# Kernel tuning notes

Hardware: AMD Instinct MI355X
Metric: run time of the kernel (lower is better)

The kernel has to match this reference:

```python
import jax, jax.numpy as jnp
import numpy as np

D_MODEL = 512
N_HEADS = 8
D_HEAD = D_MODEL // N_HEADS
EPS = 1e-5


def layer_norm(x, g, b):
    mu = jnp.mean(x, axis=-1, keepdims=True)
    var = jnp.mean(jnp.square(x - mu), axis=-1, keepdims=True)
    return (x - mu) * jax.lax.rsqrt(var + EPS) * g + b


def setup_inputs() -> dict:
    key = jax.random.key(0)
    ks = jax.random.split(key, 8)
    B, L, D = 2, 4096, D_MODEL
    x = jax.random.normal(ks[0], (B, L, D), dtype=jnp.float32)
    # monotonically increasing event timestamps (hours)
    timestamps = jnp.sort(jax.random.uniform(ks[1], (B, L), dtype=jnp.float32) * 1000.0, axis=-1)
    mask = jnp.ones((B, L), dtype=jnp.float32)
    s = 0.02
    return {
        "x": x,
        "timestamps": timestamps,
        "mask": mask,
        "ln1_g": jnp.ones((D,), jnp.float32),
        "ln1_b": jnp.zeros((D,), jnp.float32),
        "w_qkv": jax.random.normal(ks[2], (3 * D, D), jnp.float32) * s,
        "w_out": jax.random.normal(ks[3], (D, D), jnp.float32) * s,
        "decay_rate": jnp.ones((N_HEADS,), jnp.float32) * 0.01,
        "ln2_g": jnp.ones((D,), jnp.float32),
        "ln2_b": jnp.zeros((D,), jnp.float32),
        "w_ff1": jax.random.normal(ks[4], (4 * D, D), jnp.float32) * s,
        "w_ff2": jax.random.normal(ks[5], (D, 4 * D), jnp.float32) * s,
    }


def reference(x, timestamps, mask, ln1_g, ln1_b, w_qkv, w_out, decay_rate, ln2_g, ln2_b, w_ff1, w_ff2):
    B, L, D = x.shape
    H, dh = N_HEADS, D_HEAD
    scale = dh ** (-0.5)

    xn = layer_norm(x, ln1_g, ln1_b)
    qkv = (xn @ w_qkv.T).reshape(B, L, 3, H, dh).transpose(2, 0, 3, 1, 4)  # [3,B,H,L,dh]
    q, k, v = qkv[0], qkv[1], qkv[2]

    attn = jnp.einsum("bhid,bhjd->bhij", q, k) * scale  # [B,H,L,L]

    # temporal-decay bias
    t_diff = jnp.abs(timestamps[:, None, :, None] - timestamps[:, None, None, :]) / 24.0  # [B,1,L,L]
    decay = jax.nn.softplus(decay_rate)[None, :, None, None]  # [1,H,1,1]
    attn = attn - decay * t_diff

    # causal mask
    causal = jnp.triu(jnp.ones((L, L), dtype=bool), k=1)
    attn = jnp.where(causal[None, None], -jnp.inf, attn)

    # padding mask over keys
    pad = (mask == 0)[:, None, None, :]  # [B,1,1,L]
    attn = jnp.where(pad, -jnp.inf, attn)

    attn = jax.nn.softmax(attn, axis=-1)
    out = jnp.einsum("bhij,bhjd->bhid", attn, v).transpose(0, 2, 1, 3).reshape(B, L, D)

    x = x + out @ w_out.T
    h = layer_norm(x, ln2_g, ln2_b)
    x = x + jax.nn.silu(h @ w_ff1.T) @ w_ff2.T
    return x
```

## Files before the change

### kernel.cpp

```cpp
#include <hip/hip_runtime.h>
#include <hip/hip_bf16.h>
#include <cmath>


#define L_SEQ 4096
#define D_MODEL 512
#define N_HEADS 8
#define D_HEAD 64
#define QKV_LD 1536

typedef __attribute__((ext_vector_type(8))) short bf16x8;
typedef __attribute__((ext_vector_type(4))) float f32x4;
typedef __attribute__((ext_vector_type(4))) unsigned u32x4;

__device__ __forceinline__ __hip_bfloat16 f2bf(float v) { return __float2bfloat16(v); }

__device__ __forceinline__ void gl_lds16(const __hip_bfloat16* g, __hip_bfloat16* l) {
  __builtin_amdgcn_global_load_lds((__attribute__((address_space(1))) void*)g,
                                   (__attribute__((address_space(3))) void*)l, 16, 0, 0);
}

__global__ __launch_bounds__(256) void cvt4_kernel(const float* __restrict__ s0, __hip_bfloat16* __restrict__ d0,
                                                   const float* __restrict__ s1, __hip_bfloat16* __restrict__ d1,
                                                   const float* __restrict__ s2, __hip_bfloat16* __restrict__ d2,
                                                   const float* __restrict__ s3, __hip_bfloat16* __restrict__ d3) {
  const int i = blockIdx.x * 256 + threadIdx.x;
  const float* s;
  __hip_bfloat16* d;
  int off;
  if (i < 196608) { s = s0; d = d0; off = i; }
  else if (i < 262144) { s = s1; d = d1; off = i - 196608; }
  else if (i < 524288) { s = s2; d = d2; off = i - 262144; }
  else { s = s3; d = d3; off = i - 524288; }
  const float4 v = ((const float4*)s)[off];
  d[4 * off + 0] = f2bf(v.x);
  d[4 * off + 1] = f2bf(v.y);
  d[4 * off + 2] = f2bf(v.z);
  d[4 * off + 3] = f2bf(v.w);
}

__global__ __launch_bounds__(256) void bias_kernel(const float* __restrict__ ts,
                                                   const float* __restrict__ mask,
                                                   const float* __restrict__ decay_rate,
                                                   float* __restrict__ biasH) {
  const int idx = blockIdx.x * 256 + threadIdx.x;
  const int col = idx & 4095;
  const int h = (idx >> 12) & 7;
  const int b = idx >> 15;
  const float LOG2E = 1.4426950408889634f;
  const float dfac = log1pf(expf(decay_rate[h])) * (1.0f / 24.0f) * LOG2E;
  const float m = mask[b * 4096 + col];
  biasH[idx] = dfac * ts[b * 4096 + col] + (m != 0.f ? 0.f : -1e30f);
}

__global__ __launch_bounds__(256) void ln_kernel(const float* __restrict__ x,
                                                 const float* __restrict__ g,
                                                 const float* __restrict__ b,
                                                 __hip_bfloat16* __restrict__ out) {
  const int row = blockIdx.x;
  const int t = threadIdx.x;
  const float* xr = x + (size_t)row * D_MODEL;
  float v0 = xr[t];
  float v1 = xr[t + 256];
  float s = v0 + v1;
  float qq = v0 * v0 + v1 * v1;
  for (int off = 32; off > 0; off >>= 1) {
    s += __shfl_xor(s, off);
    qq += __shfl_xor(qq, off);
  }
  __shared__ float red[8];
  const int wid = t >> 6;
  if ((t & 63) == 0) { red[wid] = s; red[4 + wid] = qq; }
  __syncthreads();
  s = red[0] + red[1] + red[2] + red[3];
  qq = red[4] + red[5] + red[6] + red[7];
  const float mu = s * (1.0f / 512.0f);
  const float var = fmaxf(qq * (1.0f / 512.0f) - mu * mu, 0.0f);
  const float rstd = rsqrtf(var + 1e-5f);
  __hip_bfloat16* orow = out + (size_t)row * D_MODEL;
  orow[t] = f2bf((v0 - mu) * rstd * g[t] + b[t]);
  orow[t + 256] = f2bf((v1 - mu) * rstd * g[t + 256] + b[t + 256]);
}

__global__ __launch_bounds__(256) void vtrans_kernel(const __hip_bfloat16* __restrict__ qkv,
                                                     __hip_bfloat16* __restrict__ vt) {
  const int gid = blockIdx.x * 256 + threadIdx.x;
  const int l = gid & 4095;
  const int bg = gid >> 12;
  const int b = bg >> 6, g = bg & 63;
  const int h = g >> 3, dg = (g & 7) * 8;
  const __hip_bfloat16* src = qkv + (size_t)(b * L_SEQ + l) * QKV_LD + 1024 + h * 64 + dg;
  bf16x8 v = *(const bf16x8*)src;
  const int kin = l & 63;
  const int sl = (kin & 0x23) | ((kin & 0x10) >> 2) | ((kin & 0x0c) << 1);
  const size_t dbase = (size_t)((b * 8 + h) * 64 + dg) * L_SEQ + (l & ~63) + sl;
  for (int j = 0; j < 8; j++)
    vt[dbase + (size_t)j * L_SEQ] = ((const __hip_bfloat16*)&v)[j];
}

template <int EPI>
__global__ __launch_bounds__(256) void gemm_kernel(const __hip_bfloat16* __restrict__ A,
                                                   const __hip_bfloat16* __restrict__ B,
                                                   int M, int N, int K,
                                                   const float* __restrict__ aux,
                                                   void* __restrict__ C) {
  __shared__ __align__(16) __hip_bfloat16 As[2][128 * 32];
  __shared__ __align__(16) __hip_bfloat16 Bs[2][128 * 32];
  const int tid = threadIdx.x;
  const int lane = tid & 63, w = tid >> 6;
  const int m0 = blockIdx.y * 128, n0 = blockIdx.x * 128;
  const int wm = (w >> 1) * 64, wn = (w & 1) * 64;
  const int r = lane & 15, q = lane >> 4;

  f32x4 acc[4][4];
  const f32x4 zz = {0.f, 0.f, 0.f, 0.f};
  for (int i = 0; i < 4; i++)
    for (int j = 0; j < 4; j++) acc[i][j] = zz;

  const int c0 = tid, c1 = 256 + tid;
  const int row0 = c0 >> 2, kb0 = (c0 & 3) * 8;
  const int row1 = c1 >> 2, kb1 = (c1 & 3) * 8;

#define GEMM_STAGE(k0, buf)                                                     \
  do {                                                                          \
    gl_lds16(A + (size_t)(m0 + row0) * K + ((k0) + kb0), &As[buf][c0 * 8]);     \
    gl_lds16(B + (size_t)(n0 + row0) * K + ((k0) + kb0), &Bs[buf][c0 * 8]);     \
    gl_lds16(A + (size_t)(m0 + row1) * K + ((k0) + kb1), &As[buf][c1 * 8]);     \
    gl_lds16(B + (size_t)(n0 + row1) * K + ((k0) + kb1), &Bs[buf][c1 * 8]);     \
  } while (0)

  GEMM_STAGE(0, 0);
  const int niter = K >> 5;
  for (int it = 0; it < niter; it++) {
    const int cur = it & 1;
    if (it + 1 < niter) {
      GEMM_STAGE((it + 1) << 5, cur ^ 1);
      asm volatile("s_waitcnt vmcnt(4)" ::: "memory");
    } else {
      asm volatile("s_waitcnt vmcnt(0)" ::: "memory");
    }
    __builtin_amdgcn_s_barrier();
    bf16x8 af[4], bfr[4];
    for (int mi = 0; mi < 4; mi++)
      af[mi] = *(const bf16x8*)(&As[cur][(wm + mi * 16 + r) * 32 + q * 8]);
    for (int ni = 0; ni < 4; ni++)
      bfr[ni] = *(const bf16x8*)(&Bs[cur][(wn + ni * 16 + r) * 32 + q * 8]);
    for (int mi = 0; mi < 4; mi++)
      for (int ni = 0; ni < 4; ni++)
        acc[mi][ni] = __builtin_amdgcn_mfma_f32_16x16x32_bf16(af[mi], bfr[ni], acc[mi][ni], 0, 0, 0);
    __builtin_amdgcn_s_barrier();
  }
#undef GEMM_STAGE

  for (int mi = 0; mi < 4; mi++)
    for (int ni = 0; ni < 4; ni++)
      for (int j = 0; j < 4; j++) {
        const int gm = m0 + wm + mi * 16 + q * 4 + j;
        const int gn = n0 + wn + ni * 16 + r;
        float v = acc[mi][ni][j];
        const size_t idx = (size_t)gm * N + gn;
        if (EPI == 0) {
          ((__hip_bfloat16*)C)[idx] = f2bf(v);
        } else if (EPI == 1) {
          ((float*)C)[idx] = v + aux[idx];
        } else if (EPI == 2) {
          v = v / (1.0f + expf(-v));
          ((__hip_bfloat16*)C)[idx] = f2bf(v);
        } else {
          ((float*)C)[idx] = v + aux[idx];
        }
      }
}

__device__ __forceinline__ void stage_kv(int w, int lane, int key0,
                                         const __hip_bfloat16* __restrict__ Kg,
                                         const __hip_bfloat16* __restrict__ Vg,
                                         __hip_bfloat16* Ks, __hip_bfloat16* Vs) {
  const int row_in = lane >> 3;
  const int cs = (lane & 7) ^ row_in;
#pragma unroll
  for (int ii = 0; ii < 2; ii++) {
    const int i = w * 2 + ii;
    const int row = i * 8 + row_in;
    gl_lds16(Kg + (size_t)(key0 + row) * QKV_LD + cs * 8, Ks + i * 512 + lane * 8);
    gl_lds16(Vg + (size_t)row * L_SEQ + key0 + cs * 8, Vs + i * 512 + lane * 8);
  }
}

template <bool CAUSAL>
__device__ __forceinline__ void attn_tile(int key0, int lw0, int r, int q,
                                          const __hip_bfloat16* Ks,
                                          const __hip_bfloat16* Vs,
                                          const float* __restrict__ biasHp,
                                          float scale2,
                                          const bf16x8& qf0, const bf16x8& qf1,
                                          f32x4* o, float& ls) {
  const int r7 = r & 7;
  const f32x4 zz = {0.f, 0.f, 0.f, 0.f};
  f32x4 bias4[4];
#pragma unroll
  for (int hc = 0; hc < 4; hc++)
    bias4[hc] = *(const f32x4*)(biasHp + key0 + hc * 16 + q * 4);
  f32x4 s[4];
  __builtin_amdgcn_s_setprio(1);
#pragma unroll
  for (int hc = 0; hc < 4; hc++) {
    const __hip_bfloat16* kr = Ks + (hc * 16 + r) * 64;
    bf16x8 k0 = *(const bf16x8*)(kr + ((q ^ r7) * 8));
    bf16x8 k1 = *(const bf16x8*)(kr + (((q + 4) ^ r7) * 8));
    f32x4 a = zz;
    a = __builtin_amdgcn_mfma_f32_16x16x32_bf16(k0, qf0, a, 0, 0, 0);
    a = __builtin_amdgcn_mfma_f32_16x16x32_bf16(k1, qf1, a, 0, 0, 0);
    s[hc] = a;
  }
  __builtin_amdgcn_s_setprio(0);
  float p[4][4];
  float sum = 0.f;
#pragma unroll
  for (int hc = 0; hc < 4; hc++)
#pragma unroll
    for (int j = 0; j < 4; j++) {
      const float v = fmaf(s[hc][j], scale2, bias4[hc][j]);
      float pv = exp2f(v);
      if (CAUSAL) pv = (key0 + hc * 16 + q * 4 + j <= lw0 + r) ? pv : 0.f;
      p[hc][j] = pv;
      sum += pv;
    }
  ls += sum;
  bf16x8 pa[2];
#pragma unroll
  for (int kc = 0; kc < 2; kc++) {
    u32x4 pw;
    unsigned w0, w1, w2, w3;
    asm("v_cvt_pk_bf16_f32 %0, %1, %2" : "=v"(w0) : "v"(p[2 * kc][0]), "v"(p[2 * kc][1]));
    asm("v_cvt_pk_bf16_f32 %0, %1, %2" : "=v"(w1) : "v"(p[2 * kc][2]), "v"(p[2 * kc][3]));
    asm("v_cvt_pk_bf16_f32 %0, %1, %2" : "=v"(w2) : "v"(p[2 * kc + 1][0]), "v"(p[2 * kc + 1][1]));
    asm("v_cvt_pk_bf16_f32 %0, %1, %2" : "=v"(w3) : "v"(p[2 * kc + 1][2]), "v"(p[2 * kc + 1][3]));
    pw[0] = w0; pw[1] = w1; pw[2] = w2; pw[3] = w3;
    pa[kc] = *(bf16x8*)&pw;
  }
  __builtin_amdgcn_s_setprio(1);
#pragma unroll
  for (int kc = 0; kc < 2; kc++)
#pragma unroll
    for (int c = 0; c < 4; c++) {
      const __hip_bfloat16* vr = Vs + (c * 16 + r) * 64 + (((kc * 4 + q) ^ r7) * 8);
      bf16x8 vf = *(const bf16x8*)vr;
      o[c] = __builtin_amdgcn_mfma_f32_16x16x32_bf16(pa[kc], vf, o[c], 0, 0, 0);
    }
  __builtin_amdgcn_s_setprio(0);
}

__global__ __launch_bounds__(256, 4) void attn_kernel(const __hip_bfloat16* __restrict__ qkv,
                                                      const __hip_bfloat16* __restrict__ vt,
                                                      const float* __restrict__ biasH,
                                                      __hip_bfloat16* __restrict__ out) {
  const int blk = blockIdx.x;
  const int g = blk >> 4;
  const int bh = blk & 15;
  const int gm = g >> 4, gk = g & 15;
  const int qi = (gm == 0) ? gk : (gm == 1) ? 63 - gk : (gm == 2) ? 16 + gk : 47 - gk;
  const int b = bh >> 3, h = bh & 7;
  const int l0 = qi * 64;
  const int tid = threadIdx.x, lane = tid & 63, w = tid >> 6;
  const int lw0 = l0 + w * 16;
  const int r = lane & 15, q = lane >> 4;

  __shared__ __align__(16) __hip_bfloat16 Ksm[2][64 * 64];
  __shared__ __align__(16) __hip_bfloat16 Vsm[2][64 * 64];

  const float LOG2E = 1.4426950408889634f;
  const float scale2 = 0.125f * LOG2E;

  const __hip_bfloat16* Kg = qkv + (size_t)b * L_SEQ * QKV_LD + 512 + h * 64;
  const __hip_bfloat16* Vg = vt + (size_t)bh * 64 * L_SEQ;
  const float* biasHp = biasH + (size_t)bh * L_SEQ;

  stage_kv(w, lane, 0, Kg, Vg, Ksm[0], Vsm[0]);

  bf16x8 qf0, qf1;
  {
    const __hip_bfloat16* qrow = qkv + (size_t)(b * L_SEQ + lw0 + r) * QKV_LD + h * 64 + q * 8;
    qf0 = *(const bf16x8*)qrow;
    qf1 = *(const bf16x8*)(qrow + 32);
  }

  const f32x4 zz = {0.f, 0.f, 0.f, 0.f};
  f32x4 o[4];
  for (int c = 0; c < 4; c++) o[c] = zz;
  float ls = 0.f;

  const int ntiles = qi + 1;
  for (int t = 0; t < ntiles; t++) {
    const int cur = t & 1;
    if (t + 1 < ntiles) {
      stage_kv(w, lane, (t + 1) << 6, Kg, Vg, Ksm[cur ^ 1], Vsm[cur ^ 1]);
      asm volatile("s_waitcnt vmcnt(4)" ::: "memory");
    } else {
      asm volatile("s_waitcnt vmcnt(0)" ::: "memory");
    }
    __builtin_amdgcn_s_barrier();
    if (t < ntiles - 1)
      attn_tile<false>(t << 6, lw0, r, q, Ksm[cur], Vsm[cur], biasHp, scale2, qf0, qf1, o, ls);
    else
      attn_tile<true>(t << 6, lw0, r, q, Ksm[cur], Vsm[cur], biasHp, scale2, qf0, qf1, o, ls);
    __builtin_amdgcn_s_barrier();
  }

  float lt = ls;
  lt += __shfl_xor(lt, 16);
  lt += __shfl_xor(lt, 32);
  const float invr = 1.0f / lt;
  float invj[4];
  for (int j = 0; j < 4; j++) invj[j] = __shfl(invr, q * 4 + j);
  for (int c = 0; c < 4; c++)
    for (int j = 0; j < 4; j++) {
      const int rowg = lw0 + q * 4 + j;
      out[(size_t)(b * L_SEQ + rowg) * D_MODEL + h * 64 + c * 16 + r] = f2bf(o[c][j] * invj[j]);
    }
}

extern "C" void kernel_launch(void* const* d_in, const int* in_sizes, int n_in,
                              void* d_out, int out_size, void* d_ws, size_t ws_size,
                              hipStream_t stream) {
  const float* x = (const float*)d_in[0];
  const float* ts = (const float*)d_in[1];
  const float* mask = (const float*)d_in[2];
  const float* ln1_g = (const float*)d_in[3];
  const float* ln1_b = (const float*)d_in[4];
  const float* w_qkv = (const float*)d_in[5];
  const float* w_out = (const float*)d_in[6];
  const float* decay = (const float*)d_in[7];
  const float* ln2_g = (const float*)d_in[8];
  const float* ln2_b = (const float*)d_in[9];
  const float* w_ff1 = (const float*)d_in[10];
  const float* w_ff2 = (const float*)d_in[11];

  char* ws = (char*)d_ws;
  __hip_bfloat16* wqkv_b = (__hip_bfloat16*)(ws + 0);
  __hip_bfloat16* wout_b = (__hip_bfloat16*)(ws + 1572864);
  __hip_bfloat16* wff1_b = (__hip_bfloat16*)(ws + 2097152);
  __hip_bfloat16* wff2_b = (__hip_bfloat16*)(ws + 4194304);
  __hip_bfloat16* xn = (__hip_bfloat16*)(ws + 6291456);
  __hip_bfloat16* vt = (__hip_bfloat16*)(ws + 6291456);
  __hip_bfloat16* qkv = (__hip_bfloat16*)(ws + 14680064);
  __hip_bfloat16* attnout = (__hip_bfloat16*)(ws + 39845888);
  __hip_bfloat16* h = attnout;
  __hip_bfloat16* ff1out = (__hip_bfloat16*)(ws + 6291456);
  float* x2 = (float*)(ws + 48234496);
  float* biasH = (float*)(ws + 48234496);
  float* out = (float*)d_out;

  const int M = 2 * L_SEQ;

  cvt4_kernel<<<dim3(3072), dim3(256), 0, stream>>>(w_qkv, wqkv_b, w_out, wout_b,
                                                    w_ff1, wff1_b, w_ff2, wff2_b);
  bias_kernel<<<dim3(256), dim3(256), 0, stream>>>(ts, mask, decay, biasH);

  ln_kernel<<<dim3(M), dim3(256), 0, stream>>>(x, ln1_g, ln1_b, xn);
  gemm_kernel<0><<<dim3(12, 64), dim3(256), 0, stream>>>(xn, wqkv_b, M, 1536, 512, nullptr, qkv);
  vtrans_kernel<<<dim3(2048), dim3(256), 0, stream>>>(qkv, vt);
  attn_kernel<<<dim3(1024), dim3(256), 0, stream>>>(qkv, vt, biasH, attnout);
  gemm_kernel<1><<<dim3(4, 64), dim3(256), 0, stream>>>(attnout, wout_b, M, 512, 512, x, x2);
  ln_kernel<<<dim3(M), dim3(256), 0, stream>>>(x2, ln2_g, ln2_b, h);
  gemm_kernel<2><<<dim3(16, 64), dim3(256), 0, stream>>>(h, wff1_b, M, 2048, 512, nullptr, ff1out);
  gemm_kernel<3><<<dim3(4, 64), dim3(256), 0, stream>>>(ff1out, wff2_b, M, 512, 2048, x2, out);
}
```

Before: 307.3 us.

## Pair causal query tiles per attention block and add 64-row residual GEMM

The attention kernel now gives each block two query tiles, qi and 63-qi, and processes them back to back. Every block therefore does the same total amount of causal work, and the grid shrinks from 1024 to 512 blocks with launch bounds relaxed to 2 blocks per CU. A new 64x128-tile GEMM with a residual epilogue replaces the 128-tile version for the out-projection and FF2, which doubles the block count on these narrow N=512 GEMMs to fill more CUs. The trade-off is fewer attention blocks in flight, and a first-tile loop that prefetches tile 0 on its final iteration for the second pass.

```diff
diff --git a/kernel.cpp b/kernel.cpp
--- a/kernel.cpp
+++ b/kernel.cpp
@@ -161,14 +161,73 @@
         const size_t idx = (size_t)gm * N + gn;
         if (EPI == 0) {
           ((__hip_bfloat16*)C)[idx] = f2bf(v);
-        } else if (EPI == 1) {
-          ((float*)C)[idx] = v + aux[idx];
-        } else if (EPI == 2) {
+        } else {
           v = v / (1.0f + expf(-v));
           ((__hip_bfloat16*)C)[idx] = f2bf(v);
-        } else {
-          ((float*)C)[idx] = v + aux[idx];
         }
+      }
+}
+
+__global__ __launch_bounds__(256) void gemm_res64_kernel(const __hip_bfloat16* __restrict__ A,
+                                                         const __hip_bfloat16* __restrict__ B,
+                                                         int M, int N, int K,
+                                                         const float* __restrict__ aux,
+                                                         float* __restrict__ C) {
+  __shared__ __align__(16) __hip_bfloat16 As[2][64 * 32];
+  __shared__ __align__(16) __hip_bfloat16 Bs[2][128 * 32];
+  const int tid = threadIdx.x;
+  const int lane = tid & 63, w = tid >> 6;
+  const int m0 = blockIdx.y * 64, n0 = blockIdx.x * 128;
+  const int wm = (w >> 1) * 32, wn = (w & 1) * 64;
+  const int r = lane & 15, q = lane >> 4;
+
+  f32x4 acc[2][4];
+  const f32x4 zz = {0.f, 0.f, 0.f, 0.f};
+  for (int i = 0; i < 2; i++)
+    for (int j = 0; j < 4; j++) acc[i][j] = zz;
+
+  const int rowA = tid >> 2, kbA = (tid & 3) * 8;
+  const int c0 = tid, c1 = 256 + tid;
+  const int rowB0 = c0 >> 2, kb0 = (c0 & 3) * 8;
+  const int rowB1 = c1 >> 2, kb1 = (c1 & 3) * 8;
+
+#define GEMM_STAGE64(k0, buf)                                                    \
+  do {                                                                           \
+    gl_lds16(A + (size_t)(m0 + rowA) * K + ((k0) + kbA), &As[buf][tid * 8]);     \
+    gl_lds16(B + (size_t)(n0 + rowB0) * K + ((k0) + kb0), &Bs[buf][c0 * 8]);     \
+    gl_lds16(B + (size_t)(n0 + rowB1) * K + ((k0) + kb1), &Bs[buf][c1 * 8]);     \
+  } while (0)
+
+  GEMM_STAGE64(0, 0);
+  const int niter = K >> 5;
+  for (int it = 0; it < niter; it++) {
+    const int cur = it & 1;
+    if (it + 1 < niter) {
+      GEMM_STAGE64((it + 1) << 5, cur ^ 1);
+      asm volatile("s_waitcnt vmcnt(3)" ::: "memory");
+    } else {
+      asm volatile("s_waitcnt vmcnt(0)" ::: "memory");
+    }
+    __builtin_amdgcn_s_barrier();
+    bf16x8 af[2], bfr[4];
+    for (int mi = 0; mi < 2; mi++)
+      af[mi] = *(const bf16x8*)(&As[cur][(wm + mi * 16 + r) * 32 + q * 8]);
+    for (int ni = 0; ni < 4; ni++)
+      bfr[ni] = *(const bf16x8*)(&Bs[cur][(wn + ni * 16 + r) * 32 + q * 8]);
+    for (int mi = 0; mi < 2; mi++)
+      for (int ni = 0; ni < 4; ni++)
+        acc[mi][ni] = __builtin_amdgcn_mfma_f32_16x16x32_bf16(af[mi], bfr[ni], acc[mi][ni], 0, 0, 0);
+    __builtin_amdgcn_s_barrier();
+  }
+#undef GEMM_STAGE64
+
+  for (int mi = 0; mi < 2; mi++)
+    for (int ni = 0; ni < 4; ni++)
+      for (int j = 0; j < 4; j++) {
+        const int gm = m0 + wm + mi * 16 + q * 4 + j;
+        const int gn = n0 + wn + ni * 16 + r;
+        const size_t idx = (size_t)gm * N + gn;
+        C[idx] = acc[mi][ni][j] + aux[idx];
       }
 }
 
@@ -251,19 +310,18 @@
   __builtin_amdgcn_s_setprio(0);
 }
 
-__global__ __launch_bounds__(256, 4) void attn_kernel(const __hip_bfloat16* __restrict__ qkv,
+__global__ __launch_bounds__(256, 2) void attn_kernel(const __hip_bfloat16* __restrict__ qkv,
                                                       const __hip_bfloat16* __restrict__ vt,
                                                       const float* __restrict__ biasH,
                                                       __hip_bfloat16* __restrict__ out) {
   const int blk = blockIdx.x;
-  const int g = blk >> 4;
   const int bh = blk & 15;
-  const int gm = g >> 4, gk = g & 15;
-  const int qi = (gm == 0) ? gk : (gm == 1) ? 63 - gk : (gm == 2) ? 16 + gk : 47 - gk;
+  const int pr = blk >> 4;
   const int b = bh >> 3, h = bh & 7;
-  const int l0 = qi * 64;
+  const int qiA = pr, qiB = 63 - pr;
+  const int l0A = qiA * 64, l0B = qiB * 64;
   const int tid = threadIdx.x, lane = tid & 63, w = tid >> 6;
-  const int lw0 = l0 + w * 16;
+  const int lw0A = l0A + w * 16, lw0B = l0B + w * 16;
   const int r = lane & 15, q = lane >> 4;
 
   __shared__ __align__(16) __hip_bfloat16 Ksm[2][64 * 64];
@@ -278,11 +336,14 @@
 
   stage_kv(w, lane, 0, Kg, Vg, Ksm[0], Vsm[0]);
 
-  bf16x8 qf0, qf1;
+  bf16x8 qfA0, qfA1, qfB0, qfB1;
   {
-    const __hip_bfloat16* qrow = qkv + (size_t)(b * L_SEQ + lw0 + r) * QKV_LD + h * 64 + q * 8;
-    qf0 = *(const bf16x8*)qrow;
-    qf1 = *(const bf16x8*)(qrow + 32);
+    const __hip_bfloat16* qrA = qkv + (size_t)(b * L_SEQ + lw0A + r) * QKV_LD + h * 64 + q * 8;
+    qfA0 = *(const bf16x8*)qrA;
+    qfA1 = *(const bf16x8*)(qrA + 32);
+    const __hip_bfloat16* qrB = qkv + (size_t)(b * L_SEQ + lw0B + r) * QKV_LD + h * 64 + q * 8;
+    qfB0 = *(const bf16x8*)qrB;
+    qfB1 = *(const bf16x8*)(qrB + 32);
   }
 
   const f32x4 zz = {0.f, 0.f, 0.f, 0.f};
@@ -290,34 +351,67 @@
   for (int c = 0; c < 4; c++) o[c] = zz;
   float ls = 0.f;
 
-  const int ntiles = qi + 1;
-  for (int t = 0; t < ntiles; t++) {
+  const int ntA = qiA + 1;
+  const int ntB = qiB + 1;
+
+  for (int t = 0; t < ntA; t++) {
     const int cur = t & 1;
-    if (t + 1 < ntiles) {
+    const int nxt_key0 = (t + 1 < ntA) ? ((t + 1) << 6) : 0;
+    stage_kv(w, lane, nxt_key0, Kg, Vg, Ksm[cur ^ 1], Vsm[cur ^ 1]);
+    asm volatile("s_waitcnt vmcnt(4)" ::: "memory");
+    __builtin_amdgcn_s_barrier();
+    if (t < ntA - 1)
+      attn_tile<false>(t << 6, lw0A, r, q, Ksm[cur], Vsm[cur], biasHp, scale2, qfA0, qfA1, o, ls);
+    else
+      attn_tile<true>(t << 6, lw0A, r, q, Ksm[cur], Vsm[cur], biasHp, scale2, qfA0, qfA1, o, ls);
+    __builtin_amdgcn_s_barrier();
+  }
+
+  {
+    float lt = ls;
+    lt += __shfl_xor(lt, 16);
+    lt += __shfl_xor(lt, 32);
+    const float invr = 1.0f / lt;
+    float invj[4];
+    for (int j = 0; j < 4; j++) invj[j] = __shfl(invr, q * 4 + j);
+    for (int c = 0; c < 4; c++)
+      for (int j = 0; j < 4; j++) {
+        const int rowg = lw0A + q * 4 + j;
+        out[(size_t)(b * L_SEQ + rowg) * D_MODEL + h * 64 + c * 16 + r] = f2bf(o[c][j] * invj[j]);
+      }
+    for (int c = 0; c < 4; c++) o[c] = zz;
+    ls = 0.f;
+  }
+
+  for (int t = 0; t < ntB; t++) {
+    const int cur = (ntA + t) & 1;
+    if (t + 1 < ntB) {
       stage_kv(w, lane, (t + 1) << 6, Kg, Vg, Ksm[cur ^ 1], Vsm[cur ^ 1]);
       asm volatile("s_waitcnt vmcnt(4)" ::: "memory");
     } else {
       asm volatile("s_waitcnt vmcnt(0)" ::: "memory");
     }
     __builtin_amdgcn_s_barrier();
-    if (t < ntiles - 1)
-      attn_tile<false>(t << 6, lw0, r, q, Ksm[cur], Vsm[cur], biasHp, scale2, qf0, qf1, o, ls);
+    if (t < ntB - 1)
+      attn_tile<false>(t << 6, lw0B, r, q, Ksm[cur], Vsm[cur], biasHp, scale2, qfB0, qfB1, o, ls);
     else
-      attn_tile<true>(t << 6, lw0, r, q, Ksm[cur], Vsm[cur], biasHp, scale2, qf0, qf1, o, ls);
-    __builtin_amdgcn_s_barrier();
-  }
-
-  float lt = ls;
-  lt += __shfl_xor(lt, 16);
-  lt += __shfl_xor(lt, 32);
-  const float invr = 1.0f / lt;
-  float invj[4];
-  for (int j = 0; j < 4; j++) invj[j] = __shfl(invr, q * 4 + j);
-  for (int c = 0; c < 4; c++)
-    for (int j = 0; j < 4; j++) {
-      const int rowg = lw0 + q * 4 + j;
-      out[(size_t)(b * L_SEQ + rowg) * D_MODEL + h * 64 + c * 16 + r] = f2bf(o[c][j] * invj[j]);
-    }
+      attn_tile<true>(t << 6, lw0B, r, q, Ksm[cur], Vsm[cur], biasHp, scale2, qfB0, qfB1, o, ls);
+    __builtin_amdgcn_s_barrier();
+  }
+
+  {
+    float lt = ls;
+    lt += __shfl_xor(lt, 16);
+    lt += __shfl_xor(lt, 32);
+    const float invr = 1.0f / lt;
+    float invj[4];
+    for (int j = 0; j < 4; j++) invj[j] = __shfl(invr, q * 4 + j);
+    for (int c = 0; c < 4; c++)
+      for (int j = 0; j < 4; j++) {
+        const int rowg = lw0B + q * 4 + j;
+        out[(size_t)(b * L_SEQ + rowg) * D_MODEL + h * 64 + c * 16 + r] = f2bf(o[c][j] * invj[j]);
+      }
+  }
 }
 
 extern "C" void kernel_launch(void* const* d_in, const int* in_sizes, int n_in,
@@ -360,9 +454,9 @@
   ln_kernel<<<dim3(M), dim3(256), 0, stream>>>(x, ln1_g, ln1_b, xn);
   gemm_kernel<0><<<dim3(12, 64), dim3(256), 0, stream>>>(xn, wqkv_b, M, 1536, 512, nullptr, qkv);
   vtrans_kernel<<<dim3(2048), dim3(256), 0, stream>>>(qkv, vt);
-  attn_kernel<<<dim3(1024), dim3(256), 0, stream>>>(qkv, vt, biasH, attnout);
-  gemm_kernel<1><<<dim3(4, 64), dim3(256), 0, stream>>>(attnout, wout_b, M, 512, 512, x, x2);
+  attn_kernel<<<dim3(512), dim3(256), 0, stream>>>(qkv, vt, biasH, attnout);
+  gemm_res64_kernel<<<dim3(4, 128), dim3(256), 0, stream>>>(attnout, wout_b, M, 512, 512, x, x2);
   ln_kernel<<<dim3(M), dim3(256), 0, stream>>>(x2, ln2_g, ln2_b, h);
   gemm_kernel<2><<<dim3(16, 64), dim3(256), 0, stream>>>(h, wff1_b, M, 2048, 512, nullptr, ff1out);
-  gemm_kernel<3><<<dim3(4, 64), dim3(256), 0, stream>>>(ff1out, wff2_b, M, 512, 2048, x2, out);
-}
+  gemm_res64_kernel<<<dim3(4, 128), dim3(256), 0, stream>>>(ff1out, wff2_b, M, 512, 2048, x2, out);
+}
```

After: 302.6 us. No clear change (-1.5%).
